# Optimization experiments

Measured on AMD Instinct MI355X. Metric: run time of the kernel, lower is better.

Reference implementation:

```python
import jax, jax.numpy as jnp
import numpy as np

N = 100000   # nodes
E = 1600000  # edges per snapshot
S = 4        # snapshots
D = 128      # node_dim
H = 256      # hidden dim
P = 10000    # post nodes


def setup_inputs() -> dict:
    key = jax.random.key(0)
    ks = jax.random.split(key, 11)
    return {
        "node_features": jax.random.normal(ks[0], (N, D), jnp.float32),
        "edge_index": jax.random.randint(ks[1], (S, 2, E), 0, N, dtype=jnp.int32),
        "post_idx": jax.random.randint(ks[2], (P,), 0, N, dtype=jnp.int32),
        "W1": jax.random.normal(ks[3], (D, H), jnp.float32) * (1.0 / np.sqrt(D)),
        "b1": jnp.zeros((H,), jnp.float32),
        "W2": jax.random.normal(ks[4], (H, H), jnp.float32) * (1.0 / np.sqrt(H)),
        "b2": jnp.zeros((H,), jnp.float32),
        "Wc1": jax.random.normal(ks[5], (H, H // 2), jnp.float32) * (1.0 / np.sqrt(H)),
        "bc1": jnp.zeros((H // 2,), jnp.float32),
        "Wc2": jax.random.normal(ks[6], (H // 2, 1), jnp.float32) * (1.0 / np.sqrt(H // 2)),
        "bc2": jnp.zeros((1,), jnp.float32),
    }


def _gcn_conv(x, W, b, src, dst):
    # PyG GCNConv: linear transform, then symmetric-normalized aggregation
    # with self-loops: out_i = sum_j (xW)_j / sqrt(d_i d_j) + (xW)_i / d_i + b
    xw = x @ W                                   # [N, H]
    deg = jnp.ones((N,), xw.dtype).at[dst].add(1.0)  # in-degree + self-loop
    dinv = jax.lax.rsqrt(deg)                    # [N]
    norm = dinv[src] * dinv[dst]                 # [E]
    msg = xw[src] * norm[:, None]                # [E, H] gather + scale
    agg = jax.ops.segment_sum(msg, dst, num_segments=N)  # scatter-add
    agg = agg + xw * (dinv * dinv)[:, None]      # self-loop term
    return agg + b


def reference(node_features, edge_index, post_idx, W1, b1, W2, b2, Wc1, bc1, Wc2, bc2):
    embs = []
    for s in range(S):  # small fixed snapshot loop
        src, dst = edge_index[s, 0], edge_index[s, 1]
        # layer 0: 128->256, relu (dropout identity in eval), no residual (dim change)
        h = jax.nn.relu(_gcn_conv(node_features, W1, b1, src, dst))
        # layer 1 (last): no relu, residual since dims match
        h = _gcn_conv(h, W2, b2, src, dst) + h
        embs.append(h)
    agg = jnp.mean(jnp.stack(embs), axis=0)      # 'mean' snapshot aggregation
    post = agg[post_idx]                         # [P, H]
    hid = jax.nn.relu(post @ Wc1 + bc1)
    logits = (hid @ Wc2 + bc2)[:, 0]
    return jax.nn.sigmoid(logits)
```

## Files before the change

kernel.cpp:

```cpp
#include <hip/hip_runtime.h>
#include <math.h>

#define N_NODES 100000
#define E_EDGES 1600000
#define S_SNAP  4
#define D_IN    128
#define H_DIM   256
#define P_POST  10000
#define SCAN_NBLK ((N_NODES + 255) / 256)
#define NBIN 8
#define BIN_W (N_NODES / NBIN)
#define FILL_CHUNK 2048
#define FILL_NCHUNK ((E_EDGES + FILL_CHUNK - 1) / FILL_CHUNK)

typedef __attribute__((ext_vector_type(8))) short bf16x8;
typedef __attribute__((ext_vector_type(4))) float f32x4;

__device__ __forceinline__ float bf2f(unsigned short u) {
    union { unsigned int i; float f; } v; v.i = ((unsigned int)u) << 16; return v.f;
}
__device__ __forceinline__ unsigned short f2bf(float f) {
    union { float f; unsigned int i; } v; v.f = f;
    unsigned int lsb = (v.i >> 16) & 1u;
    v.i += 0x7fffu + lsb;
    return (unsigned short)(v.i >> 16);
}

__global__ void zero32_kernel(unsigned int* __restrict__ p, int n) {
    int i = blockIdx.x * blockDim.x + threadIdx.x;
    if (i < n) p[i] = 0u;
}

__global__ void hist_kernel(const int* __restrict__ dst, int* __restrict__ deg,
        int* __restrict__ slot) {
    int i = blockIdx.x * blockDim.x + threadIdx.x;
    if (i < E_EDGES) slot[i] = atomicAdd(&deg[dst[i]], 1);
}

__global__ __launch_bounds__(256) void scan_part_kernel(const int* __restrict__ deg,
        int* __restrict__ bsum, float* __restrict__ dinv) {
    __shared__ int red[4];
    int i = blockIdx.x * 256 + threadIdx.x;
    int s = 0;
    if (i < N_NODES) {
        s = deg[i];
        dinv[i] = rsqrtf((float)(s + 1));
    }
    int t = s;
    #pragma unroll
    for (int off = 32; off > 0; off >>= 1) t += __shfl_down(t, off, 64);
    int wave = threadIdx.x >> 6, lane = threadIdx.x & 63;
    if (lane == 0) red[wave] = t;
    __syncthreads();
    if (threadIdx.x == 0) bsum[blockIdx.x] = red[0] + red[1] + red[2] + red[3];
}

__global__ __launch_bounds__(512) void scan_top_kernel(const int* __restrict__ bsum,
        int* __restrict__ boff) {
    __shared__ int s[512];
    int t = threadIdx.x;
    s[t] = (t < SCAN_NBLK) ? bsum[t] : 0;
    __syncthreads();
    for (int off = 1; off < 512; off <<= 1) {
        int v = (t >= off) ? s[t - off] : 0;
        __syncthreads();
        s[t] += v;
        __syncthreads();
    }
    if (t < SCAN_NBLK) boff[t] = (t == 0) ? 0 : s[t - 1];
}

__global__ __launch_bounds__(256) void scan_fin_kernel(const int* __restrict__ deg,
        const int* __restrict__ boff, int* __restrict__ rowptr) {
    __shared__ int s[256];
    int b = blockIdx.x, t = threadIdx.x;
    int i = b * 256 + t;
    int v = (i < N_NODES) ? deg[i] : 0;
    s[t] = v;
    __syncthreads();
    for (int off = 1; off < 256; off <<= 1) {
        int u = (t >= off) ? s[t - off] : 0;
        __syncthreads();
        s[t] += u;
        __syncthreads();
    }
    if (i < N_NODES) rowptr[i] = boff[b] + s[t] - v;
    if (i == 0) rowptr[N_NODES] = E_EDGES;
}

__global__ __launch_bounds__(256) void fill_kernel(const int* __restrict__ src,
        const int* __restrict__ dst, const int* __restrict__ slot,
        const int* __restrict__ rowptr, int* __restrict__ csrsrc) {
    int chunk = blockIdx.x >> 3;
    int bin = blockIdx.x & (NBIN - 1);
    int lo = bin * BIN_W, hi = lo + BIN_W;
    int base = chunk * FILL_CHUNK + threadIdx.x;
    #pragma unroll
    for (int k = 0; k < FILL_CHUNK / 256; ++k) {
        int i = base + k * 256;
        if (i < E_EDGES) {
            int d = dst[i];
            if (d >= lo && d < hi) csrsrc[rowptr[d] + slot[i]] = src[i];
        }
    }
}

__global__ __launch_bounds__(256) void gemm_xw1_mfma(const float* __restrict__ A,
        const float* __restrict__ B, unsigned short* __restrict__ C, int M) {
    __shared__ unsigned short As[64][136];
    __shared__ unsigned short Bs[64][136];
    int tid = threadIdx.x;
    int m0 = blockIdx.x * 64, n0 = blockIdx.y * 64;
    {
        int row = tid >> 2, c0 = (tid & 3) * 32;
        int gm = m0 + row;
        #pragma unroll
        for (int i = 0; i < 8; ++i) {
            float4 v = make_float4(0.f, 0.f, 0.f, 0.f);
            if (gm < M) v = *(const float4*)(A + (size_t)gm * D_IN + c0 + i * 4);
            As[row][c0 + i * 4 + 0] = f2bf(v.x);
            As[row][c0 + i * 4 + 1] = f2bf(v.y);
            As[row][c0 + i * 4 + 2] = f2bf(v.z);
            As[row][c0 + i * 4 + 3] = f2bf(v.w);
        }
    }
    {
        int k = tid >> 1, nb = (tid & 1) * 32;
        #pragma unroll
        for (int i = 0; i < 8; ++i) {
            float4 v = *(const float4*)(B + (size_t)k * H_DIM + n0 + nb + i * 4);
            Bs[nb + i * 4 + 0][k] = f2bf(v.x);
            Bs[nb + i * 4 + 1][k] = f2bf(v.y);
            Bs[nb + i * 4 + 2][k] = f2bf(v.z);
            Bs[nb + i * 4 + 3][k] = f2bf(v.w);
        }
    }
    __syncthreads();
    int w = tid >> 6, l = tid & 63;
    int q = l >> 4, mrow = l & 15;
    f32x4 acc[4] = {{0.f,0.f,0.f,0.f},{0.f,0.f,0.f,0.f},{0.f,0.f,0.f,0.f},{0.f,0.f,0.f,0.f}};
    #pragma unroll
    for (int kk = 0; kk < 4; ++kk) {
        bf16x8 a = *(const bf16x8*)&As[16 * w + mrow][kk * 32 + q * 8];
        #pragma unroll
        for (int ct = 0; ct < 4; ++ct) {
            bf16x8 b = *(const bf16x8*)&Bs[ct * 16 + mrow][kk * 32 + q * 8];
            acc[ct] = __builtin_amdgcn_mfma_f32_16x16x32_bf16(a, b, acc[ct], 0, 0, 0);
        }
    }
    #pragma unroll
    for (int ct = 0; ct < 4; ++ct) {
        int col = n0 + ct * 16 + mrow;
        #pragma unroll
        for (int i = 0; i < 4; ++i) {
            int m = m0 + 16 * w + q * 4 + i;
            if (m < M) C[(size_t)m * H_DIM + col] = f2bf(acc[ct][i]);
        }
    }
}

__global__ __launch_bounds__(256) void spmm_l0_kernel(const unsigned short* __restrict__ xw1,
        const float* __restrict__ dinv, const int* __restrict__ rowptr,
        const int* __restrict__ csrsrc, const float* __restrict__ b1,
        unsigned short* __restrict__ h) {
    int r = (blockIdx.x << 2) + (threadIdx.x >> 6);
    int lane = threadIdx.x & 63;
    int e0 = rowptr[r], e1 = rowptr[r + 1];
    float di = dinv[r];
    float4 acc = make_float4(0.f, 0.f, 0.f, 0.f);
    const ushort4* tp = (const ushort4*)xw1;
    int e = e0;
    for (; e + 4 <= e1; e += 4) {
        int s0 = csrsrc[e], s1 = csrsrc[e + 1], s2 = csrsrc[e + 2], s3 = csrsrc[e + 3];
        float w0 = dinv[s0] * di, w1 = dinv[s1] * di, w2 = dinv[s2] * di, w3 = dinv[s3] * di;
        ushort4 u0 = tp[(size_t)s0 * 64 + lane];
        ushort4 u1 = tp[(size_t)s1 * 64 + lane];
        ushort4 u2 = tp[(size_t)s2 * 64 + lane];
        ushort4 u3 = tp[(size_t)s3 * 64 + lane];
        acc.x = fmaf(bf2f(u0.x), w0, acc.x); acc.y = fmaf(bf2f(u0.y), w0, acc.y);
        acc.z = fmaf(bf2f(u0.z), w0, acc.z); acc.w = fmaf(bf2f(u0.w), w0, acc.w);
        acc.x = fmaf(bf2f(u1.x), w1, acc.x); acc.y = fmaf(bf2f(u1.y), w1, acc.y);
        acc.z = fmaf(bf2f(u1.z), w1, acc.z); acc.w = fmaf(bf2f(u1.w), w1, acc.w);
        acc.x = fmaf(bf2f(u2.x), w2, acc.x); acc.y = fmaf(bf2f(u2.y), w2, acc.y);
        acc.z = fmaf(bf2f(u2.z), w2, acc.z); acc.w = fmaf(bf2f(u2.w), w2, acc.w);
        acc.x = fmaf(bf2f(u3.x), w3, acc.x); acc.y = fmaf(bf2f(u3.y), w3, acc.y);
        acc.z = fmaf(bf2f(u3.z), w3, acc.z); acc.w = fmaf(bf2f(u3.w), w3, acc.w);
    }
    for (; e < e1; ++e) {
        int s = csrsrc[e];
        float wv = dinv[s] * di;
        ushort4 u = tp[(size_t)s * 64 + lane];
        acc.x = fmaf(bf2f(u.x), wv, acc.x); acc.y = fmaf(bf2f(u.y), wv, acc.y);
        acc.z = fmaf(bf2f(u.z), wv, acc.z); acc.w = fmaf(bf2f(u.w), wv, acc.w);
    }
    ushort4 us = tp[(size_t)r * 64 + lane];
    float wd = di * di;
    float4 bb = ((const float4*)b1)[lane];
    ushort4 o;
    o.x = f2bf(fmaxf(fmaf(bf2f(us.x), wd, acc.x) + bb.x, 0.f));
    o.y = f2bf(fmaxf(fmaf(bf2f(us.y), wd, acc.y) + bb.y, 0.f));
    o.z = f2bf(fmaxf(fmaf(bf2f(us.z), wd, acc.z) + bb.z, 0.f));
    o.w = f2bf(fmaxf(fmaf(bf2f(us.w), wd, acc.w) + bb.w, 0.f));
    ((ushort4*)h)[(size_t)r * 64 + lane] = o;
}

__global__ __launch_bounds__(256) void spmm_h_post_kernel(const unsigned short* __restrict__ h,
        const float* __restrict__ dinv, const int* __restrict__ rowptr,
        const int* __restrict__ csrsrc, const int* __restrict__ post,
        float* __restrict__ t1p) {
    int p = (blockIdx.x << 2) + (threadIdx.x >> 6);
    int lane = threadIdx.x & 63;
    int r = post[p];
    int e0 = rowptr[r], e1 = rowptr[r + 1];
    float di = dinv[r];
    float4 acc = make_float4(0.f, 0.f, 0.f, 0.f);
    const ushort4* hp = (const ushort4*)h;
    int e = e0;
    for (; e + 4 <= e1; e += 4) {
        int s0 = csrsrc[e], s1 = csrsrc[e + 1], s2 = csrsrc[e + 2], s3 = csrsrc[e + 3];
        float w0 = dinv[s0] * di, w1 = dinv[s1] * di, w2 = dinv[s2] * di, w3 = dinv[s3] * di;
        ushort4 u0 = hp[(size_t)s0 * 64 + lane];
        ushort4 u1 = hp[(size_t)s1 * 64 + lane];
        ushort4 u2 = hp[(size_t)s2 * 64 + lane];
        ushort4 u3 = hp[(size_t)s3 * 64 + lane];
        acc.x = fmaf(bf2f(u0.x), w0, acc.x); acc.y = fmaf(bf2f(u0.y), w0, acc.y);
        acc.z = fmaf(bf2f(u0.z), w0, acc.z); acc.w = fmaf(bf2f(u0.w), w0, acc.w);
        acc.x = fmaf(bf2f(u1.x), w1, acc.x); acc.y = fmaf(bf2f(u1.y), w1, acc.y);
        acc.z = fmaf(bf2f(u1.z), w1, acc.z); acc.w = fmaf(bf2f(u1.w), w1, acc.w);
        acc.x = fmaf(bf2f(u2.x), w2, acc.x); acc.y = fmaf(bf2f(u2.y), w2, acc.y);
        acc.z = fmaf(bf2f(u2.z), w2, acc.z); acc.w = fmaf(bf2f(u2.w), w2, acc.w);
        acc.x = fmaf(bf2f(u3.x), w3, acc.x); acc.y = fmaf(bf2f(u3.y), w3, acc.y);
        acc.z = fmaf(bf2f(u3.z), w3, acc.z); acc.w = fmaf(bf2f(u3.w), w3, acc.w);
    }
    for (; e < e1; ++e) {
        int s = csrsrc[e];
        float wv = dinv[s] * di;
        ushort4 u = hp[(size_t)s * 64 + lane];
        acc.x = fmaf(bf2f(u.x), wv, acc.x); acc.y = fmaf(bf2f(u.y), wv, acc.y);
        acc.z = fmaf(bf2f(u.z), wv, acc.z); acc.w = fmaf(bf2f(u.w), wv, acc.w);
    }
    ushort4 u = hp[(size_t)r * 64 + lane];
    float wd = di * di;
    acc.x = fmaf(bf2f(u.x), wd, acc.x);
    acc.y = fmaf(bf2f(u.y), wd, acc.y);
    acc.z = fmaf(bf2f(u.z), wd, acc.z);
    acc.w = fmaf(bf2f(u.w), wd, acc.w);
    ((float4*)t1p)[(size_t)p * 64 + lane] = acc;
}

__global__ __launch_bounds__(256) void gemm_l1_mfma(const float* __restrict__ A,
        const float* __restrict__ B, const float* __restrict__ b2,
        const unsigned short* __restrict__ h, const int* __restrict__ post,
        float* __restrict__ accP, int M) {
    __shared__ unsigned short As[64][136];
    __shared__ unsigned short Bs[64][136];
    int tid = threadIdx.x;
    int m0 = blockIdx.x * 64, n0 = blockIdx.y * 64;
    int w = tid >> 6, l = tid & 63;
    int q = l >> 4, mrow = l & 15;
    f32x4 acc[4] = {{0.f,0.f,0.f,0.f},{0.f,0.f,0.f,0.f},{0.f,0.f,0.f,0.f},{0.f,0.f,0.f,0.f}};
    for (int kk = 0; kk < 256; kk += 128) {
        __syncthreads();
        {
            int row = tid >> 2, c0 = (tid & 3) * 32;
            int gm = m0 + row;
            #pragma unroll
            for (int i = 0; i < 8; ++i) {
                float4 v = make_float4(0.f, 0.f, 0.f, 0.f);
                if (gm < M) v = *(const float4*)(A + (size_t)gm * 256 + kk + c0 + i * 4);
                As[row][c0 + i * 4 + 0] = f2bf(v.x);
                As[row][c0 + i * 4 + 1] = f2bf(v.y);
                As[row][c0 + i * 4 + 2] = f2bf(v.z);
                As[row][c0 + i * 4 + 3] = f2bf(v.w);
            }
        }
        {
            int k = tid >> 1, nb = (tid & 1) * 32;
            #pragma unroll
            for (int i = 0; i < 8; ++i) {
                float4 v = *(const float4*)(B + (size_t)(kk + k) * H_DIM + n0 + nb + i * 4);
                Bs[nb + i * 4 + 0][k] = f2bf(v.x);
                Bs[nb + i * 4 + 1][k] = f2bf(v.y);
                Bs[nb + i * 4 + 2][k] = f2bf(v.z);
                Bs[nb + i * 4 + 3][k] = f2bf(v.w);
            }
        }
        __syncthreads();
        #pragma unroll
        for (int ks = 0; ks < 4; ++ks) {
            bf16x8 a = *(const bf16x8*)&As[16 * w + mrow][ks * 32 + q * 8];
            #pragma unroll
            for (int ct = 0; ct < 4; ++ct) {
                bf16x8 b = *(const bf16x8*)&Bs[ct * 16 + mrow][ks * 32 + q * 8];
                acc[ct] = __builtin_amdgcn_mfma_f32_16x16x32_bf16(a, b, acc[ct], 0, 0, 0);
            }
        }
    }
    #pragma unroll
    for (int ct = 0; ct < 4; ++ct) {
        int col = n0 + ct * 16 + mrow;
        float bias = b2[col];
        #pragma unroll
        for (int i = 0; i < 4; ++i) {
            int m = m0 + 16 * w + q * 4 + i;
            if (m < M) {
                int node = post[m];
                float hv = bf2f(h[(size_t)node * 256 + col]);
                accP[(size_t)m * 256 + col] += acc[ct][i] + bias + hv;
            }
        }
    }
}

__global__ __launch_bounds__(128) void classifier_kernel(const float* __restrict__ accP,
        const float* __restrict__ Wc1, const float* __restrict__ bc1,
        const float* __restrict__ Wc2, const float* __restrict__ bc2,
        float* __restrict__ out) {
    __shared__ float arow[8][256];
    __shared__ float red[2][8];
    int p0 = blockIdx.x << 3;
    int tid = threadIdx.x;
    for (int idx = tid; idx < 8 * 256; idx += 128) {
        int pl = idx >> 8, k = idx & 255;
        arow[pl][k] = 0.25f * accP[(size_t)(p0 + pl) * 256 + k];
    }
    __syncthreads();
    float s[8];
    float b = bc1[tid];
    #pragma unroll
    for (int pl = 0; pl < 8; ++pl) s[pl] = b;
    for (int k = 0; k < 256; ++k) {
        float wv = Wc1[k * 128 + tid];
        #pragma unroll
        for (int pl = 0; pl < 8; ++pl) s[pl] = fmaf(arow[pl][k], wv, s[pl]);
    }
    float wc2 = Wc2[tid];
    float part[8];
    #pragma unroll
    for (int pl = 0; pl < 8; ++pl) part[pl] = fmaxf(s[pl], 0.f) * wc2;
    #pragma unroll
    for (int off = 32; off > 0; off >>= 1)
        #pragma unroll
        for (int pl = 0; pl < 8; ++pl) part[pl] += __shfl_down(part[pl], off, 64);
    int wave = tid >> 6, lane = tid & 63;
    if (lane == 0) {
        #pragma unroll
        for (int pl = 0; pl < 8; ++pl) red[wave][pl] = part[pl];
    }
    __syncthreads();
    if (tid < 8) {
        float logit = red[0][tid] + red[1][tid] + bc2[0];
        out[p0 + tid] = 1.f / (1.f + expf(-logit));
    }
}

extern "C" void kernel_launch(void* const* d_in, const int* in_sizes, int n_in,
                              void* d_out, int out_size, void* d_ws, size_t ws_size,
                              hipStream_t stream) {
    const float* x   = (const float*)d_in[0];
    const int*   ei  = (const int*)d_in[1];
    const int*   post= (const int*)d_in[2];
    const float* W1  = (const float*)d_in[3];
    const float* b1  = (const float*)d_in[4];
    const float* W2  = (const float*)d_in[5];
    const float* b2  = (const float*)d_in[6];
    const float* Wc1 = (const float*)d_in[7];
    const float* bc1 = (const float*)d_in[8];
    const float* Wc2 = (const float*)d_in[9];
    const float* bc2 = (const float*)d_in[10];
    float* out = (float*)d_out;

    char* w = (char*)d_ws;
    size_t off = 0;
#define WS_ALLOC(type, name, count) \
    type* name = (type*)(w + off); \
    off += (((size_t)(count) * sizeof(type)) + 255) & ~(size_t)255;
    WS_ALLOC(unsigned short, xw1,  (size_t)N_NODES * H_DIM)
    WS_ALLOC(unsigned short, hbuf, (size_t)N_NODES * H_DIM)
    WS_ALLOC(float,          t1p,  (size_t)P_POST * H_DIM)
    WS_ALLOC(float,          accP, (size_t)P_POST * H_DIM)
    WS_ALLOC(int,            deg,    N_NODES)
    WS_ALLOC(float,          dinvb,  N_NODES)
    WS_ALLOC(int,            rowptr, N_NODES + 1)
    WS_ALLOC(int,            csrsrc, E_EDGES)
    WS_ALLOC(int,            bsum,   SCAN_NBLK)
    WS_ALLOC(int,            boff,   SCAN_NBLK)
#undef WS_ALLOC
    int* slot = (int*)t1p;
    (void)ws_size; (void)in_sizes; (void)n_in; (void)out_size;

    zero32_kernel<<<(P_POST * H_DIM + 255) / 256, 256, 0, stream>>>((unsigned int*)accP, P_POST * H_DIM);

    dim3 gg((N_NODES + 63) / 64, H_DIM / 64);
    gemm_xw1_mfma<<<gg, 256, 0, stream>>>(x, W1, xw1, N_NODES);

    for (int s = 0; s < S_SNAP; ++s) {
        const int* srcs = ei + (size_t)s * 2 * E_EDGES;
        const int* dsts = srcs + E_EDGES;
        zero32_kernel<<<(N_NODES + 255) / 256, 256, 0, stream>>>((unsigned int*)deg, N_NODES);
        hist_kernel<<<E_EDGES / 256, 256, 0, stream>>>(dsts, deg, slot);
        scan_part_kernel<<<SCAN_NBLK, 256, 0, stream>>>(deg, bsum, dinvb);
        scan_top_kernel<<<1, 512, 0, stream>>>(bsum, boff);
        scan_fin_kernel<<<SCAN_NBLK, 256, 0, stream>>>(deg, boff, rowptr);
        fill_kernel<<<FILL_NCHUNK * NBIN, 256, 0, stream>>>(srcs, dsts, slot, rowptr, csrsrc);
        spmm_l0_kernel<<<N_NODES / 4, 256, 0, stream>>>(xw1, dinvb, rowptr, csrsrc, b1, hbuf);
        spmm_h_post_kernel<<<P_POST / 4, 256, 0, stream>>>(hbuf, dinvb, rowptr, csrsrc, post, t1p);
        dim3 g1((P_POST + 63) / 64, H_DIM / 64);
        gemm_l1_mfma<<<g1, 256, 0, stream>>>(t1p, W2, b2, hbuf, post, accP, P_POST);
    }
    classifier_kernel<<<P_POST / 8, 128, 0, stream>>>(accP, Wc1, bc1, Wc2, bc2, out);
}
```

Baseline: 1.332 ms.

## Batch CSR construction for all snapshots into single hist/scan/fill passes

Graph preprocessing (degree histogram, prefix scan, CSR fill) now runs once over all four snapshots using concatenated per-snapshot degree, rowptr and CSR arrays, instead of six kernels per snapshot inside the loop. The SpMM kernels take a snapshot offset to index the combined arrays. The scan kernels also process four nodes per thread with vector loads. This removes about twenty small kernel launches and their serialization, and gives the preprocessing kernels larger grids. In exchange, workspace grows to hold four snapshots of CSR data, and the hbuf buffer is reused as slot storage.

```diff
diff --git a/kernel.cpp b/kernel.cpp
--- a/kernel.cpp
+++ b/kernel.cpp
@@ -7,11 +7,13 @@
 #define D_IN    128
 #define H_DIM   256
 #define P_POST  10000
-#define SCAN_NBLK ((N_NODES + 255) / 256)
+#define N4 (S_SNAP * N_NODES)
+#define E4 (S_SNAP * E_EDGES)
+#define NBLK4 ((N4 + 1023) / 1024)
 #define NBIN 8
 #define BIN_W (N_NODES / NBIN)
 #define FILL_CHUNK 2048
-#define FILL_NCHUNK ((E_EDGES + FILL_CHUNK - 1) / FILL_CHUNK)
+#define FILL_NCHUNK ((E4 + FILL_CHUNK - 1) / FILL_CHUNK)
 
 typedef __attribute__((ext_vector_type(8))) short bf16x8;
 typedef __attribute__((ext_vector_type(4))) float f32x4;
@@ -31,22 +33,28 @@
     if (i < n) p[i] = 0u;
 }
 
-__global__ void hist_kernel(const int* __restrict__ dst, int* __restrict__ deg,
-        int* __restrict__ slot) {
-    int i = blockIdx.x * blockDim.x + threadIdx.x;
-    if (i < E_EDGES) slot[i] = atomicAdd(&deg[dst[i]], 1);
-}
-
-__global__ __launch_bounds__(256) void scan_part_kernel(const int* __restrict__ deg,
-        int* __restrict__ bsum, float* __restrict__ dinv) {
+__global__ void hist4_kernel(const int* __restrict__ ei, int* __restrict__ deg4,
+        int* __restrict__ slot4) {
+    int i = blockIdx.x * 256 + threadIdx.x;
+    int s = i / E_EDGES;
+    int j = i - s * E_EDGES;
+    int d = ei[(size_t)s * 2 * E_EDGES + E_EDGES + j];
+    slot4[i] = atomicAdd(&deg4[s * N_NODES + d], 1);
+}
+
+__global__ __launch_bounds__(256) void scan_part4_kernel(const int* __restrict__ deg4,
+        int* __restrict__ bsum, float* __restrict__ dinv4) {
     __shared__ int red[4];
-    int i = blockIdx.x * 256 + threadIdx.x;
-    int s = 0;
-    if (i < N_NODES) {
-        s = deg[i];
-        dinv[i] = rsqrtf((float)(s + 1));
-    }
-    int t = s;
+    int base = blockIdx.x * 1024 + threadIdx.x * 4;
+    int4 v = make_int4(0, 0, 0, 0);
+    if (base < N4) {
+        v = *(const int4*)(deg4 + base);
+        dinv4[base + 0] = rsqrtf((float)(v.x + 1));
+        dinv4[base + 1] = rsqrtf((float)(v.y + 1));
+        dinv4[base + 2] = rsqrtf((float)(v.z + 1));
+        dinv4[base + 3] = rsqrtf((float)(v.w + 1));
+    }
+    int t = v.x + v.y + v.z + v.w;
     #pragma unroll
     for (int off = 32; off > 0; off >>= 1) t += __shfl_down(t, off, 64);
     int wave = threadIdx.x >> 6, lane = threadIdx.x & 63;
@@ -59,7 +67,7 @@
         int* __restrict__ boff) {
     __shared__ int s[512];
     int t = threadIdx.x;
-    s[t] = (t < SCAN_NBLK) ? bsum[t] : 0;
+    s[t] = (t < NBLK4) ? bsum[t] : 0;
     __syncthreads();
     for (int off = 1; off < 512; off <<= 1) {
         int v = (t >= off) ? s[t - off] : 0;
@@ -67,30 +75,39 @@
         s[t] += v;
         __syncthreads();
     }
-    if (t < SCAN_NBLK) boff[t] = (t == 0) ? 0 : s[t - 1];
-}
-
-__global__ __launch_bounds__(256) void scan_fin_kernel(const int* __restrict__ deg,
-        const int* __restrict__ boff, int* __restrict__ rowptr) {
-    __shared__ int s[256];
-    int b = blockIdx.x, t = threadIdx.x;
-    int i = b * 256 + t;
-    int v = (i < N_NODES) ? deg[i] : 0;
-    s[t] = v;
+    if (t < NBLK4) boff[t] = (t == 0) ? 0 : s[t - 1];
+}
+
+__global__ __launch_bounds__(256) void scan_fin4_kernel(const int* __restrict__ deg4,
+        const int* __restrict__ boff, int* __restrict__ rowptr4) {
+    __shared__ int sh[256];
+    int base = blockIdx.x * 1024 + threadIdx.x * 4;
+    int4 v = make_int4(0, 0, 0, 0);
+    if (base < N4) v = *(const int4*)(deg4 + base);
+    int tsum = v.x + v.y + v.z + v.w;
+    sh[threadIdx.x] = tsum;
     __syncthreads();
     for (int off = 1; off < 256; off <<= 1) {
-        int u = (t >= off) ? s[t - off] : 0;
-        __syncthreads();
-        s[t] += u;
-        __syncthreads();
-    }
-    if (i < N_NODES) rowptr[i] = boff[b] + s[t] - v;
-    if (i == 0) rowptr[N_NODES] = E_EDGES;
-}
-
-__global__ __launch_bounds__(256) void fill_kernel(const int* __restrict__ src,
-        const int* __restrict__ dst, const int* __restrict__ slot,
-        const int* __restrict__ rowptr, int* __restrict__ csrsrc) {
+        int u = (threadIdx.x >= off) ? sh[threadIdx.x - off] : 0;
+        __syncthreads();
+        sh[threadIdx.x] += u;
+        __syncthreads();
+    }
+    int excl = boff[blockIdx.x] + sh[threadIdx.x] - tsum;
+    if (base < N4) {
+        int4 o;
+        o.x = excl;
+        o.y = excl + v.x;
+        o.z = excl + v.x + v.y;
+        o.w = excl + v.x + v.y + v.z;
+        *(int4*)(rowptr4 + base) = o;
+    }
+    if (base == 0) rowptr4[N4] = E4;
+}
+
+__global__ __launch_bounds__(256) void fill4_kernel(const int* __restrict__ ei,
+        const int* __restrict__ slot4, const int* __restrict__ rowptr4,
+        int* __restrict__ csrsrc4) {
     int chunk = blockIdx.x >> 3;
     int bin = blockIdx.x & (NBIN - 1);
     int lo = bin * BIN_W, hi = lo + BIN_W;
@@ -98,9 +115,14 @@
     #pragma unroll
     for (int k = 0; k < FILL_CHUNK / 256; ++k) {
         int i = base + k * 256;
-        if (i < E_EDGES) {
-            int d = dst[i];
-            if (d >= lo && d < hi) csrsrc[rowptr[d] + slot[i]] = src[i];
+        if (i < E4) {
+            int s = i / E_EDGES;
+            int j = i - s * E_EDGES;
+            int d = ei[(size_t)s * 2 * E_EDGES + E_EDGES + j];
+            if (d >= lo && d < hi) {
+                int sc = ei[(size_t)s * 2 * E_EDGES + j];
+                csrsrc4[rowptr4[s * N_NODES + d] + slot4[i]] = sc;
+            }
         }
     }
 }
@@ -160,19 +182,21 @@
 }
 
 __global__ __launch_bounds__(256) void spmm_l0_kernel(const unsigned short* __restrict__ xw1,
-        const float* __restrict__ dinv, const int* __restrict__ rowptr,
-        const int* __restrict__ csrsrc, const float* __restrict__ b1,
-        unsigned short* __restrict__ h) {
+        const float* __restrict__ dinv4, const int* __restrict__ rowptr4,
+        const int* __restrict__ csrsrc4, const float* __restrict__ b1,
+        unsigned short* __restrict__ h, int soff) {
     int r = (blockIdx.x << 2) + (threadIdx.x >> 6);
     int lane = threadIdx.x & 63;
-    int e0 = rowptr[r], e1 = rowptr[r + 1];
-    float di = dinv[r];
+    int rg = soff + r;
+    int e0 = rowptr4[rg], e1 = rowptr4[rg + 1];
+    float di = dinv4[rg];
     float4 acc = make_float4(0.f, 0.f, 0.f, 0.f);
     const ushort4* tp = (const ushort4*)xw1;
+    const float* dv = dinv4 + soff;
     int e = e0;
     for (; e + 4 <= e1; e += 4) {
-        int s0 = csrsrc[e], s1 = csrsrc[e + 1], s2 = csrsrc[e + 2], s3 = csrsrc[e + 3];
-        float w0 = dinv[s0] * di, w1 = dinv[s1] * di, w2 = dinv[s2] * di, w3 = dinv[s3] * di;
+        int s0 = csrsrc4[e], s1 = csrsrc4[e + 1], s2 = csrsrc4[e + 2], s3 = csrsrc4[e + 3];
+        float w0 = dv[s0] * di, w1 = dv[s1] * di, w2 = dv[s2] * di, w3 = dv[s3] * di;
         ushort4 u0 = tp[(size_t)s0 * 64 + lane];
         ushort4 u1 = tp[(size_t)s1 * 64 + lane];
         ushort4 u2 = tp[(size_t)s2 * 64 + lane];
@@ -187,8 +211,8 @@
         acc.z = fmaf(bf2f(u3.z), w3, acc.z); acc.w = fmaf(bf2f(u3.w), w3, acc.w);
     }
     for (; e < e1; ++e) {
-        int s = csrsrc[e];
-        float wv = dinv[s] * di;
+        int s = csrsrc4[e];
+        float wv = dv[s] * di;
         ushort4 u = tp[(size_t)s * 64 + lane];
         acc.x = fmaf(bf2f(u.x), wv, acc.x); acc.y = fmaf(bf2f(u.y), wv, acc.y);
         acc.z = fmaf(bf2f(u.z), wv, acc.z); acc.w = fmaf(bf2f(u.w), wv, acc.w);
@@ -205,20 +229,22 @@
 }
 
 __global__ __launch_bounds__(256) void spmm_h_post_kernel(const unsigned short* __restrict__ h,
-        const float* __restrict__ dinv, const int* __restrict__ rowptr,
-        const int* __restrict__ csrsrc, const int* __restrict__ post,
-        float* __restrict__ t1p) {
+        const float* __restrict__ dinv4, const int* __restrict__ rowptr4,
+        const int* __restrict__ csrsrc4, const int* __restrict__ post,
+        float* __restrict__ t1p, int soff) {
     int p = (blockIdx.x << 2) + (threadIdx.x >> 6);
     int lane = threadIdx.x & 63;
     int r = post[p];
-    int e0 = rowptr[r], e1 = rowptr[r + 1];
-    float di = dinv[r];
+    int rg = soff + r;
+    int e0 = rowptr4[rg], e1 = rowptr4[rg + 1];
+    float di = dinv4[rg];
     float4 acc = make_float4(0.f, 0.f, 0.f, 0.f);
     const ushort4* hp = (const ushort4*)h;
+    const float* dv = dinv4 + soff;
     int e = e0;
     for (; e + 4 <= e1; e += 4) {
-        int s0 = csrsrc[e], s1 = csrsrc[e + 1], s2 = csrsrc[e + 2], s3 = csrsrc[e + 3];
-        float w0 = dinv[s0] * di, w1 = dinv[s1] * di, w2 = dinv[s2] * di, w3 = dinv[s3] * di;
+        int s0 = csrsrc4[e], s1 = csrsrc4[e + 1], s2 = csrsrc4[e + 2], s3 = csrsrc4[e + 3];
+        float w0 = dv[s0] * di, w1 = dv[s1] * di, w2 = dv[s2] * di, w3 = dv[s3] * di;
         ushort4 u0 = hp[(size_t)s0 * 64 + lane];
         ushort4 u1 = hp[(size_t)s1 * 64 + lane];
         ushort4 u2 = hp[(size_t)s2 * 64 + lane];
@@ -233,8 +259,8 @@
         acc.z = fmaf(bf2f(u3.z), w3, acc.z); acc.w = fmaf(bf2f(u3.w), w3, acc.w);
     }
     for (; e < e1; ++e) {
-        int s = csrsrc[e];
-        float wv = dinv[s] * di;
+        int s = csrsrc4[e];
+        float wv = dv[s] * di;
         ushort4 u = hp[(size_t)s * 64 + lane];
         acc.x = fmaf(bf2f(u.x), wv, acc.x); acc.y = fmaf(bf2f(u.y), wv, acc.y);
         acc.z = fmaf(bf2f(u.z), wv, acc.z); acc.w = fmaf(bf2f(u.w), wv, acc.w);
@@ -375,36 +401,38 @@
 #define WS_ALLOC(type, name, count) \
     type* name = (type*)(w + off); \
     off += (((size_t)(count) * sizeof(type)) + 255) & ~(size_t)255;
-    WS_ALLOC(unsigned short, xw1,  (size_t)N_NODES * H_DIM)
-    WS_ALLOC(unsigned short, hbuf, (size_t)N_NODES * H_DIM)
-    WS_ALLOC(float,          t1p,  (size_t)P_POST * H_DIM)
-    WS_ALLOC(float,          accP, (size_t)P_POST * H_DIM)
-    WS_ALLOC(int,            deg,    N_NODES)
-    WS_ALLOC(float,          dinvb,  N_NODES)
-    WS_ALLOC(int,            rowptr, N_NODES + 1)
-    WS_ALLOC(int,            csrsrc, E_EDGES)
-    WS_ALLOC(int,            bsum,   SCAN_NBLK)
-    WS_ALLOC(int,            boff,   SCAN_NBLK)
+    WS_ALLOC(unsigned short, xw1,     (size_t)N_NODES * H_DIM)
+    WS_ALLOC(unsigned short, hbuf,    (size_t)N_NODES * H_DIM)
+    WS_ALLOC(float,          t1p,     (size_t)P_POST * H_DIM)
+    WS_ALLOC(float,          accP,    (size_t)P_POST * H_DIM)
+    WS_ALLOC(int,            deg4,    N4)
+    WS_ALLOC(float,          dinv4,   N4)
+    WS_ALLOC(int,            rowptr4, N4 + 4)
+    WS_ALLOC(int,            csrsrc4, E4)
+    WS_ALLOC(int,            bsum,    NBLK4)
+    WS_ALLOC(int,            boff,    NBLK4)
 #undef WS_ALLOC
-    int* slot = (int*)t1p;
+    int* slot4 = (int*)hbuf;
     (void)ws_size; (void)in_sizes; (void)n_in; (void)out_size;
 
-    zero32_kernel<<<(P_POST * H_DIM + 255) / 256, 256, 0, stream>>>((unsigned int*)accP, P_POST * H_DIM);
+    zero32_kernel<<<(P_POST * H_DIM + N4 + 255) / 256, 256, 0, stream>>>(
+        (unsigned int*)accP, P_POST * H_DIM + N4);
+
+    hist4_kernel<<<E4 / 256, 256, 0, stream>>>(ei, deg4, slot4);
+    scan_part4_kernel<<<NBLK4, 256, 0, stream>>>(deg4, bsum, dinv4);
+    scan_top_kernel<<<1, 512, 0, stream>>>(bsum, boff);
+    scan_fin4_kernel<<<NBLK4, 256, 0, stream>>>(deg4, boff, rowptr4);
+    fill4_kernel<<<FILL_NCHUNK * NBIN, 256, 0, stream>>>(ei, slot4, rowptr4, csrsrc4);
 
     dim3 gg((N_NODES + 63) / 64, H_DIM / 64);
     gemm_xw1_mfma<<<gg, 256, 0, stream>>>(x, W1, xw1, N_NODES);
 
     for (int s = 0; s < S_SNAP; ++s) {
-        const int* srcs = ei + (size_t)s * 2 * E_EDGES;
-        const int* dsts = srcs + E_EDGES;
-        zero32_kernel<<<(N_NODES + 255) / 256, 256, 0, stream>>>((unsigned int*)deg, N_NODES);
-        hist_kernel<<<E_EDGES / 256, 256, 0, stream>>>(dsts, deg, slot);
-        scan_part_kernel<<<SCAN_NBLK, 256, 0, stream>>>(deg, bsum, dinvb);
-        scan_top_kernel<<<1, 512, 0, stream>>>(bsum, boff);
-        scan_fin_kernel<<<SCAN_NBLK, 256, 0, stream>>>(deg, boff, rowptr);
-        fill_kernel<<<FILL_NCHUNK * NBIN, 256, 0, stream>>>(srcs, dsts, slot, rowptr, csrsrc);
-        spmm_l0_kernel<<<N_NODES / 4, 256, 0, stream>>>(xw1, dinvb, rowptr, csrsrc, b1, hbuf);
-        spmm_h_post_kernel<<<P_POST / 4, 256, 0, stream>>>(hbuf, dinvb, rowptr, csrsrc, post, t1p);
+        int soff = s * N_NODES;
+        spmm_l0_kernel<<<N_NODES / 4, 256, 0, stream>>>(xw1, dinv4, rowptr4, csrsrc4,
+                                                        b1, hbuf, soff);
+        spmm_h_post_kernel<<<P_POST / 4, 256, 0, stream>>>(hbuf, dinv4, rowptr4, csrsrc4,
+                                                           post, t1p, soff);
         dim3 g1((P_POST + 63) / 64, H_DIM / 64);
         gemm_l1_mfma<<<g1, 256, 0, stream>>>(t1p, W2, b2, hbuf, post, accP, P_POST);
     }
```

Result: faster. 1.295 ms (-2.8%).
